# Performance work log

Measured on AMD Instinct MI355X. Metric: run time of the kernel, lower is better.

Reference implementation:

```python
import jax, jax.numpy as jnp
import numpy as np
from jax import lax

D = 30   # embedding_dim (hardcoded in repo)
Q = 30   # question length
N = 4000 # number of sentences in doc
S = 100  # tokens per sentence
K = 5    # k_for_maxpool
SLOPE = 0.1  # LeakyReLU negative slope


def setup_inputs() -> dict:
    key = jax.random.key(0)
    ks = jax.random.split(key, 20)
    rn = lambda k, sh: jax.random.normal(k, sh, dtype=jnp.float32)
    ru = lambda k, sh: jax.random.uniform(k, sh, dtype=jnp.float32)
    return {
        "doc_sents_embeds": rn(ks[0], (N, S, D)),
        "sents_gaf": ru(ks[1], (N, 3)),
        "question_embeds": rn(ks[2], (Q, D)),
        "q_idfs": ru(ks[3], (Q, 1)),
        "doc_gaf": ru(ks[4], (4,)),
        "conv1_w": rn(ks[5], (D, D, 3)) * 0.1,
        "conv1_b": rn(ks[6], (D,)) * 0.1,
        "conv2_w": rn(ks[7], (D, D, 3)) * 0.1,
        "conv2_b": rn(ks[8], (D,)) * 0.1,
        "qw_W": rn(ks[9], (1, D + 1)) * 0.1,
        "qw_b": rn(ks[10], (1,)) * 0.1,
        "lq1_W": rn(ks[11], (8, 6)) * 0.1,
        "lq1_b": rn(ks[12], (8,)) * 0.1,
        "lq2_W": rn(ks[13], (1, 8)) * 0.1,
        "lq2_b": rn(ks[14], (1,)) * 0.1,
        "so_W": rn(ks[15], (1, 4)) * 0.1,
        "so_b": rn(ks[16], (1,)) * 0.1,
        "fl_W": rn(ks[17], (1, 5)) * 0.1,
        "fl_b": rn(ks[18], (1,)) * 0.1,
    }


def _leaky(x):
    return jnp.where(x >= 0, x, SLOPE * x)


def _conv_block(x, w, b):
    # x: [B, L, D]. torch Conv1d(D, D, 3, padding=2) then slice [1:L+1]
    # is exactly a 'same' conv with padding 1 on each side; then residual add.
    y = lax.conv_general_dilated(x.transpose(0, 2, 1), w, (1,), [(1, 1)],
                                 dimension_numbers=("NCH", "OIH", "NCH"))
    y = _leaky(y + b[None, :, None])
    return y.transpose(0, 2, 1) + x


def _cos_sim(A, B):
    # A: [Q, D], B: [N, S, D] -> [N, Q, S] (num/den as in torch my_cosine_sim)
    num = jnp.einsum("qd,nsd->nqs", A, B)
    den = jnp.linalg.norm(A, axis=-1)[None, :, None] * jnp.linalg.norm(B, axis=-1)[:, None, :]
    return num / den


def _pool(sim):
    # sort-based k-max pooling -> [max, avg_of_top_k]; sim: [N, Q, S] -> [N, Q, 2]
    vals = lax.top_k(sim, K)[0]  # descending
    return jnp.stack([vals[..., 0], vals.mean(-1)], axis=-1)


def reference(doc_sents_embeds, sents_gaf, question_embeds, q_idfs, doc_gaf,
              conv1_w, conv1_b, conv2_w, conv2_b, qw_W, qw_b,
              lq1_W, lq1_b, lq2_W, lq2_b, so_W, so_b, fl_W, fl_b):
    # question context (two residual trigram convs)
    q_conv = _conv_block(question_embeds[None], conv1_w, conv1_b)
    q_conv = _conv_block(q_conv, conv2_w, conv2_b)[0]          # [Q, D]
    # question term weights
    qw_in = jnp.concatenate([q_conv, q_idfs], axis=-1)          # [Q, D+1]
    q_weights = jax.nn.softmax((qw_in @ qw_W.T + qw_b)[:, 0])   # [Q]
    # sentence context convs (batched over all sentences)
    conv_res = _conv_block(doc_sents_embeds, conv1_w, conv1_b)
    conv_res = _conv_block(conv_res, conv2_w, conv2_b)          # [N, S, D]
    # similarity matrices
    sim_insens = _cos_sim(question_embeds, doc_sents_embeds)    # [N, Q, S]
    sim_oh = (sim_insens > 1.0 - 1e-3).astype(sim_insens.dtype)
    sim_sens = _cos_sim(q_conv, conv_res)
    # k-max pooling and per-q tiny MLP attention
    feats = jnp.concatenate([_pool(sim_oh), _pool(sim_insens), _pool(sim_sens)], axis=-1)  # [N, Q, 6]
    lo = _leaky(feats @ lq1_W.T + lq1_b) @ lq2_W.T + lq2_b      # [N, Q, 1]
    lo = lo[..., 0] * q_weights[None, :]
    sent_emit = lo.sum(-1) / Q                                  # [N]
    # per-sentence output layer
    sent_feats = jnp.concatenate([sents_gaf, sent_emit[:, None]], axis=-1)  # [N, 4]
    sent_scores = jax.nn.sigmoid((sent_feats @ so_W.T + so_b)[:, 0])        # [N]
    # doc-level score
    doc_rep = jnp.concatenate([jnp.max(sent_scores)[None], doc_gaf])        # [5]
    final = doc_rep @ fl_W.T + fl_b                                          # [1]
    return final, sent_scores
```

## Files before the change

kernel.cpp:

```cpp
#include <hip/hip_runtime.h>
#include <hip/hip_bf16.h>

#define SLOPE 0.1f

#define OFF_QW    1816
#define OFF_QNI   1846
#define OFF_QNS   1876
#define OFF_QNN   1906
#define OFF_B1    4606
#define OFF_B2    7336
#define OFF_LQ1W  7366
#define OFF_LQ1B  7414
#define OFF_LQ2W  7422
#define OFF_LQ2B  7430
#define OFF_SOW   7431
#define OFF_SOB   7435
#define OFF_FLW   7436
#define OFF_FLB   7441
#define U16_QEA   16384
#define U16_QCA   17408
#define U16_WB1   18432
#define U16_WB2   21504

#define XDW 1548

typedef __attribute__((ext_vector_type(8))) __bf16 bf16x8;
typedef __attribute__((ext_vector_type(4))) float f32x4;

union Frag { uint4 u4; uint u[4]; bf16x8 v; };

__device__ __forceinline__ float bf2f(ushort h) {
    union { uint u; float f; } c; c.u = ((uint)h) << 16; return c.f;
}
__device__ __forceinline__ ushort f2bf(float f) {
    union { float f; uint u; } c; c.f = f;
    uint u = c.u;
    return (ushort)((u + 0x7FFFu + ((u >> 16) & 1u)) >> 16);
}
__device__ __forceinline__ float ldx(const void* p, long i, int bf) {
    if (bf) return bf2f(((const ushort*)p)[i]);
    return ((const float*)p)[i];
}
__device__ __forceinline__ uint pk2(float lo, float hi) {
    uint r;
    asm("v_cvt_pk_bf16_f32 %0, %1, %2" : "=v"(r) : "v"(lo), "v"(hi));
    return r;
}
__device__ __forceinline__ float blo(uint u) { return __uint_as_float(u << 16); }
__device__ __forceinline__ float bhi(uint u) { return __uint_as_float(u & 0xFFFF0000u); }
__device__ __forceinline__ float lk(float x) { return fmaxf(x, SLOPE * x); }

#define CE(x, y) { float _hi = fmaxf(x, y), _lo = fminf(x, y); x = _hi; y = _lo; }

__device__ __forceinline__ void sort4d(float& a, float& b, float& c, float& d) {
    CE(a, b); CE(c, d); CE(a, c); CE(b, d); CE(b, c);
}
__device__ __forceinline__ void merge44_5(const float* a, const float* b, float* t) {
    t[0] = fmaxf(a[0], b[0]);
    t[1] = fmaxf(fminf(a[0], b[0]), fmaxf(a[1], b[1]));
    t[2] = fmaxf(fmaxf(fminf(a[0], b[1]), fminf(a[1], b[0])), fmaxf(a[2], b[2]));
    t[3] = fmaxf(fmaxf(fminf(a[0], b[2]), fminf(a[1], b[1])),
                 fmaxf(fminf(a[2], b[0]), fmaxf(a[3], b[3])));
    t[4] = fmaxf(fmaxf(fminf(a[0], b[3]), fminf(a[1], b[2])),
                 fmaxf(fminf(a[2], b[1]), fminf(a[3], b[0])));
}
__device__ __forceinline__ void merge54_5(const float* a, const float* b, float* t) {
    t[0] = fmaxf(a[0], b[0]);
    t[1] = fmaxf(fminf(a[0], b[0]), fmaxf(a[1], b[1]));
    t[2] = fmaxf(fmaxf(fminf(a[0], b[1]), fminf(a[1], b[0])), fmaxf(a[2], b[2]));
    t[3] = fmaxf(fmaxf(fminf(a[0], b[2]), fminf(a[1], b[1])),
                 fmaxf(fminf(a[2], b[0]), fmaxf(a[3], b[3])));
    t[4] = fmaxf(fmaxf(fmaxf(fminf(a[0], b[3]), fminf(a[1], b[2])),
                       fmaxf(fminf(a[2], b[1]), fminf(a[3], b[0]))), a[4]);
}
__device__ __forceinline__ void merge55_5(const float* a, const float* b, float* t) {
    t[0] = fmaxf(a[0], b[0]);
    t[1] = fmaxf(fminf(a[0], b[0]), fmaxf(a[1], b[1]));
    t[2] = fmaxf(fmaxf(fminf(a[0], b[1]), fminf(a[1], b[0])), fmaxf(a[2], b[2]));
    t[3] = fmaxf(fmaxf(fminf(a[0], b[2]), fminf(a[1], b[1])),
                 fmaxf(fminf(a[2], b[0]), fmaxf(a[3], b[3])));
    t[4] = fmaxf(fmaxf(fmaxf(fminf(a[0], b[3]), fminf(a[1], b[2])),
                       fmaxf(fminf(a[2], b[1]), fminf(a[3], b[0]))),
                 fmaxf(a[4], b[4]));
}

__device__ __forceinline__ int detect_bf(const void* doc_in, int tid, int* scnt) {
    if (tid == 0) *scnt = 0;
    __syncthreads();
    const ushort* p = (const ushort*)doc_in;
    int local = 0;
    for (int i = tid; i < 4096; i += 256) {
        unsigned e = (p[i] >> 7) & 0xFFu;
        if (e != 0u && (e < 100u || e > 134u)) local++;
    }
    atomicAdd(scnt, local);
    __syncthreads();
    return (*scnt > 200) ? 0 : 1;
}

__global__ __launch_bounds__(256) void k_prep(
        const void* doc_in,
        const void* qe_in, const void* qidf_in,
        const void* w1_in, const void* b1_in,
        const void* w2_in, const void* b2_in,
        const void* qwW_in, const void* qwb_in,
        const void* lq1W_in, const void* lq1b_in,
        const void* lq2W_in, const void* lq2b_in,
        const void* soW_in, const void* sob_in,
        const void* flW_in, const void* flb_in,
        float* ws) {
    const int tid = threadIdx.x;
    const int blk = blockIdx.x;
    __shared__ float QE[900], T1[900], QC[900], W[2700], IDF[32], LG[32];
    __shared__ int scnt;

    const int bf = detect_bf(doc_in, tid, &scnt);
    ushort* wsu = (ushort*)ws;

    if (blk == 1) {
        if (tid == 0) { ((int*)ws)[0] = bf; }
        if (tid < 30) ws[OFF_B1 + tid] = ldx(b1_in, tid, bf);
        if (tid < 48) ws[OFF_LQ1W + tid] = ldx(lq1W_in, tid, bf);
        if (tid < 8)  { ws[OFF_LQ1B + tid] = ldx(lq1b_in, tid, bf);
                        ws[OFF_LQ2W + tid] = ldx(lq2W_in, tid, bf); }
        if (tid < 4)  ws[OFF_SOW + tid] = ldx(soW_in, tid, bf);
        if (tid < 5)  ws[OFF_FLW + tid] = ldx(flW_in, tid, bf);
        if (tid == 1) { ws[OFF_LQ2B] = ldx(lq2b_in, 0, bf);
                        ws[OFF_SOB]  = ldx(sob_in, 0, bf);
                        ws[OFF_FLB]  = ldx(flb_in, 0, bf); }
        for (int i = tid; i < 3072; i += 256) {
            int o = i / 96, kk = i % 96;
            int k = kk >> 5, ii = kk & 31;
            float v1 = 0.f;
            if (o < 30 && ii < 30) v1 = ldx(w1_in, (long)o*90 + ii*3 + k, bf);
            wsu[U16_WB1 + i] = f2bf(v1);
        }
        return;
    }
    if (blk == 2) {
        if (tid < 30) ws[OFF_B2 + tid] = ldx(b2_in, tid, bf);
        for (int i = tid; i < 3072; i += 256) {
            int o = i / 96, kk = i % 96;
            int k = kk >> 5, ii = kk & 31;
            float v2 = 0.f;
            if (o < 30 && ii < 30) v2 = ldx(w2_in, (long)o*90 + ii*3 + k, bf);
            wsu[U16_WB2 + i] = f2bf(v2);
        }
        return;
    }

    if (tid == 0) { ((int*)ws)[0] = bf; }

    for (int i = tid; i < 900; i += 256) QE[i] = ldx(qe_in, i, bf);
    if (tid < 30) IDF[tid] = ldx(qidf_in, tid, bf);
    for (int i = tid; i < 2700; i += 256) W[i] = ldx(w1_in, i, bf);
    __syncthreads();

    for (int idx = tid; idx < 900; idx += 256) {
        int s = idx / 30, o = idx % 30;
        float acc = ldx(b1_in, o, bf);
        for (int k = 0; k < 3; ++k) {
            int t = s + k - 1;
            if (t < 0 || t >= 30) continue;
            for (int i = 0; i < 30; ++i) acc += QE[t*30 + i] * W[o*90 + i*3 + k];
        }
        acc = acc >= 0.f ? acc : SLOPE * acc;
        T1[idx] = acc + QE[idx];
    }
    __syncthreads();
    for (int i = tid; i < 2700; i += 256) W[i] = ldx(w2_in, i, bf);
    __syncthreads();
    for (int idx = tid; idx < 900; idx += 256) {
        int s = idx / 30, o = idx % 30;
        float acc = ldx(b2_in, o, bf);
        for (int k = 0; k < 3; ++k) {
            int t = s + k - 1;
            if (t < 0 || t >= 30) continue;
            for (int i = 0; i < 30; ++i) acc += T1[t*30 + i] * W[o*90 + i*3 + k];
        }
        acc = acc >= 0.f ? acc : SLOPE * acc;
        QC[idx] = acc + T1[idx];
    }
    __syncthreads();

    if (tid < 30) {
        float s1 = 0.f, s2 = 0.f;
        for (int d = 0; d < 30; ++d) {
            float a = QE[tid*30 + d]; s1 += a*a;
            float b = QC[tid*30 + d]; s2 += b*b;
        }
        float n1 = sqrtf(s1);
        ws[OFF_QNN + tid] = n1;
        ws[OFF_QNI + tid] = 1.0f / n1;
        ws[OFF_QNS + tid] = 1.0f / sqrtf(s2);
        float z = ldx(qwb_in, 0, bf);
        for (int d = 0; d < 30; ++d) z += QC[tid*30 + d] * ldx(qwW_in, d, bf);
        z += IDF[tid] * ldx(qwW_in, 30, bf);
        LG[tid] = z;
    }
    __syncthreads();
    if (tid == 0) {
        float m = -1e30f;
        for (int q = 0; q < 30; ++q) m = fmaxf(m, LG[q]);
        float sum = 0.f, e[30];
        for (int q = 0; q < 30; ++q) { e[q] = expf(LG[q] - m); sum += e[q]; }
        for (int q = 0; q < 30; ++q) ws[OFF_QW + q] = e[q] / sum;
    }
    for (int i = tid; i < 1024; i += 256) {
        int q = i >> 5, d = i & 31;
        float ve = (q < 30 && d < 30) ? QE[q*30 + d] : 0.f;
        float vc = (q < 30 && d < 30) ? QC[q*30 + d] : 0.f;
        wsu[U16_QEA + i] = f2bf(ve);
        wsu[U16_QCA + i] = f2bf(vc);
    }
}

__global__ __launch_bounds__(128, 4) void k_main(const void* doc_in, const void* gaf_in,
                                                 void* out, float* ws) {
    const int n = blockIdx.x;
    const int tid = threadIdx.x;
    const int bf = ((const int*)ws)[0];
    const int lane = tid & 63;
    const int wid = tid >> 6;
    const int l15 = lane & 15;
    const int quad = lane >> 4;
    const int q = wid * 16 + l15;

    __shared__ __align__(16) uint XA[XDW];
    __shared__ __align__(16) uint XB[XDW];
    __shared__ __align__(16) float INVX[112];
    __shared__ float PART[2];

    const ushort* wsu = (const ushort*)ws;
    const uint4* qeA = (const uint4*)(wsu + U16_QEA);
    const uint4* qcA = (const uint4*)(wsu + U16_QCA);
    const uint4* wb1 = (const uint4*)(wsu + U16_WB1);
    const uint4* wb2 = (const uint4*)(wsu + U16_WB2);

    float ga0 = ldx(gaf_in, (long)n*3 + 0, bf);
    float ga1 = ldx(gaf_in, (long)n*3 + 1, bf);
    float ga2 = ldx(gaf_in, (long)n*3 + 2, bf);

    if (tid < 48) {
        int j = (tid < 15) ? tid : (1500 + tid);
        XA[j] = 0u; XB[j] = 0u;
    } else if (tid < 60) {
        INVX[100 + (tid - 48)] = 0.f;
    }
    for (int g = tid; g < 400; g += 128) {
        int r = g >> 2, t = g & 3;
        int base = (r + 1) * 15 + t * 4;
        float s2;
        if (bf) {
            const uint* gp = (const uint*)doc_in + (size_t)n * 1500 + r * 15 + t * 4;
            uint a = gp[0], b = gp[1], c = gp[2];
            uint d = (t < 3) ? gp[3] : 0u;
            XA[base] = a; XA[base + 1] = b; XA[base + 2] = c;
            if (t < 3) XA[base + 3] = d;
            float x0 = blo(a), x1 = bhi(a), x2 = blo(b), x3 = bhi(b);
            float x4 = blo(c), x5 = bhi(c), x6 = blo(d), x7 = bhi(d);
            s2 = x0*x0 + x1*x1 + x2*x2 + x3*x3 + x4*x4 + x5*x5 + x6*x6 + x7*x7;
        } else {
            const float* p = (const float*)doc_in + (size_t)n * 3000 + r * 30 + t * 8;
            float2 f0 = ((const float2*)p)[0];
            float2 f1 = ((const float2*)p)[1];
            float2 f2 = ((const float2*)p)[2];
            float2 f3 = (t < 3) ? ((const float2*)p)[3] : make_float2(0.f, 0.f);
            XA[base]     = pk2(f0.x, f0.y);
            XA[base + 1] = pk2(f1.x, f1.y);
            XA[base + 2] = pk2(f2.x, f2.y);
            if (t < 3) XA[base + 3] = pk2(f3.x, f3.y);
            s2 = f0.x*f0.x + f0.y*f0.y + f1.x*f1.x + f1.y*f1.y
               + f2.x*f2.x + f2.y*f2.y + f3.x*f3.x + f3.y*f3.y;
        }
        s2 += __shfl_xor(s2, 1);
        s2 += __shfl_xor(s2, 2);
        if (t == 0) INVX[r] = 1.f / sqrtf(s2);
    }
    __syncthreads();

    auto sim_pool = [&](const uint4* qa, int iqOff, bool do_oh,
                        float& o0, float& o1, float& m0, float& m1) {
        Frag b;
        b.u4 = qa[q * 4 + quad];
        f32x4 acc[7];
        #pragma unroll
        for (int mt = 0; mt < 7; ++mt) {
            int m = mt * 16 + l15;
            Frag a;
            if (m < 100) {
                int base = (m + 1) * 15 + quad * 4;
                a.u[0] = XA[base];     a.u[1] = XA[base + 1];
                a.u[2] = XA[base + 2]; a.u[3] = XA[base + 3];
            } else { a.u[0] = a.u[1] = a.u[2] = a.u[3] = 0u; }
            f32x4 z = {0.f, 0.f, 0.f, 0.f};
            acc[mt] = __builtin_amdgcn_mfma_f32_16x16x32_bf16(a.v, b.v, z, 0, 0, 0);
        }
        const float4* INVX4 = (const float4*)INVX;
        float thr = (do_oh && q < 30) ? 0.999f * ws[OFF_QNN + q] : 1e30f;
        float iq  = (q < 30) ? ws[iqOff + q] : 0.f;
        float g[7][4];
        int cnt = 0;
        #pragma unroll
        for (int mt = 0; mt < 7; ++mt) {
            float4 ix = INVX4[mt * 4 + quad];
            float ixa[4] = {ix.x, ix.y, ix.z, ix.w};
            #pragma unroll
            for (int r = 0; r < 4; ++r) {
                float u = acc[mt][r] * ixa[r];
                if (mt == 6 && (quad * 4 + r) >= 4) u = -1e30f;
                g[mt][r] = u;
                if (do_oh) cnt += (u > thr) ? 1 : 0;
            }
        }
        #pragma unroll
        for (int mt = 0; mt < 7; ++mt) sort4d(g[mt][0], g[mt][1], g[mt][2], g[mt][3]);
        float p0[5], p1[5], p2[5], q0[5], q1[5], t[5];
        merge44_5(g[0], g[1], p0);
        merge44_5(g[2], g[3], p1);
        merge44_5(g[4], g[5], p2);
        merge55_5(p0, p1, q0);
        merge54_5(p2, g[6], q1);
        merge55_5(q0, q1, t);
        #pragma unroll
        for (int d = 16; d < 64; d <<= 1) {
            float pp[5];
            pp[0] = __shfl_xor(t[0], d); pp[1] = __shfl_xor(t[1], d);
            pp[2] = __shfl_xor(t[2], d); pp[3] = __shfl_xor(t[3], d);
            pp[4] = __shfl_xor(t[4], d);
            if (do_oh) cnt += __shfl_xor(cnt, d);
            float tn[5];
            merge55_5(t, pp, tn);
            t[0] = tn[0]; t[1] = tn[1]; t[2] = tn[2]; t[3] = tn[3]; t[4] = tn[4];
        }
        if (do_oh) {
            o0 = cnt > 0 ? 1.f : 0.f;
            o1 = (float)(cnt > 5 ? 5 : cnt) * 0.2f;
        }
        m0 = t[0] * iq;
        m1 = (t[0] + t[1] + t[2] + t[3] + t[4]) * 0.2f * iq;
    };

    auto conv_dual = [&](const uint* src, uint* dst, const uint4* wb, int bOff,
                         bool donorm) {
        const int mtb = wid ? 3 : 0;
        const int mte = wid ? 6 : 2;
        Frag wf0[3], wf1[3];
        #pragma unroll
        for (int k = 0; k < 3; ++k) {
            wf0[k].u4 = wb[l15 * 12 + k * 4 + quad];
            wf1[k].u4 = wb[(16 + l15) * 12 + k * 4 + quad];
        }
        float b40[4], b41[4];
        #pragma unroll
        for (int r = 0; r < 4; ++r) {
            int o0 = quad * 4 + r, o1 = 16 + o0;
            b40[r] = ws[bOff + o0];
            b41[r] = (o1 < 30) ? ws[bOff + o1] : 0.f;
        }
        for (int mt = mtb; mt <= mte; ++mt) {
            const int s = mt * 16 + l15;
            const bool sv = (s < 100);
            Frag f0, f1, f2;
            if (sv) {
                int base = s * 15 + quad * 4;
                f0.u[0] = src[base];      f0.u[1] = src[base + 1];
                f0.u[2] = src[base + 2];  f0.u[3] = src[base + 3];
                base += 15;
                f1.u[0] = src[base];      f1.u[1] = src[base + 1];
                f1.u[2] = src[base + 2];  f1.u[3] = src[base + 3];
                base += 15;
                f2.u[0] = src[base];      f2.u[1] = src[base + 1];
                f2.u[2] = src[base + 2];  f2.u[3] = src[base + 3];
            } else {
                f0.u[0]=f0.u[1]=f0.u[2]=f0.u[3]=0u;
                f1 = f0; f2 = f0;
            }
            const int db = (s + 1) * 15 + quad * 2;
            uint u0 = 0u, u1 = 0u, u2 = 0u, u3 = 0u;
            if (sv) {
                uint2 ua = *(const uint2*)(src + db);
                uint2 ub = *(const uint2*)(src + db + 8);
                u0 = ua.x; u1 = ua.y; u2 = ub.x; u3 = ub.y;
            }
            f32x4 a0 = {0.f, 0.f, 0.f, 0.f}, a1 = {0.f, 0.f, 0.f, 0.f};
            a0 = __builtin_amdgcn_mfma_f32_16x16x32_bf16(wf0[0].v, f0.v, a0, 0, 0, 0);
            a1 = __builtin_amdgcn_mfma_f32_16x16x32_bf16(wf1[0].v, f0.v, a1, 0, 0, 0);
            a0 = __builtin_amdgcn_mfma_f32_16x16x32_bf16(wf0[1].v, f1.v, a0, 0, 0, 0);
            a1 = __builtin_amdgcn_mfma_f32_16x16x32_bf16(wf1[1].v, f1.v, a1, 0, 0, 0);
            a0 = __builtin_amdgcn_mfma_f32_16x16x32_bf16(wf0[2].v, f2.v, a0, 0, 0, 0);
            a1 = __builtin_amdgcn_mfma_f32_16x16x32_bf16(wf1[2].v, f2.v, a1, 0, 0, 0);
            float ss = 0.f;
            if (sv) {
                float v0 = lk(a0[0] + b40[0]) + blo(u0);
                float v1 = lk(a0[1] + b40[1]) + bhi(u0);
                float v2 = lk(a0[2] + b40[2]) + blo(u1);
                float v3 = lk(a0[3] + b40[3]) + bhi(u1);
                *(uint2*)(dst + db) = make_uint2(pk2(v0, v1), pk2(v2, v3));
                float w0 = lk(a1[0] + b41[0]) + blo(u2);
                float w1 = lk(a1[1] + b41[1]) + bhi(u2);
                uint s45 = pk2(w0, w1);
                ss = v0*v0 + v1*v1 + v2*v2 + v3*v3 + w0*w0 + w1*w1;
                if (quad < 3) {
                    float w2 = lk(a1[2] + b41[2]) + blo(u3);
                    float w3 = lk(a1[3] + b41[3]) + bhi(u3);
                    *(uint2*)(dst + db + 8) = make_uint2(s45, pk2(w2, w3));
                    ss += w2*w2 + w3*w3;
                } else {
                    dst[db + 8] = s45;
                }
            }
            if (donorm) {
                ss += __shfl_xor(ss, 16);
                ss += __shfl_xor(ss, 32);
                if (quad == 0 && sv) INVX[s] = 1.f / sqrtf(ss);
            }
        }
    };

    float fe0, fe1, fe2, fe3, fe4, fe5;
    sim_pool(qeA, OFF_QNI, true, fe0, fe1, fe2, fe3);
    conv_dual(XA, XB, wb1, OFF_B1, false);
    __syncthreads();

    conv_dual(XB, XA, wb2, OFF_B2, true);
    __syncthreads();

    sim_pool(qcA, OFF_QNS, false, fe0, fe1, fe4, fe5);
    float val = 0.f;
    if (quad == 0 && q < 30) {
        float f[6] = {fe0, fe1, fe2, fe3, fe4, fe5};
        float lo = ws[OFF_LQ2B];
        #pragma unroll
        for (int j = 0; j < 8; ++j) {
            float h = ws[OFF_LQ1B + j];
            #pragma unroll
            for (int i = 0; i < 6; ++i) h += f[i] * ws[OFF_LQ1W + j*6 + i];
            h = lk(h);
            lo += h * ws[OFF_LQ2W + j];
        }
        val = lo * ws[OFF_QW + q];
    }
    #pragma unroll
    for (int d = 32; d >= 1; d >>= 1) val += __shfl_xor(val, d);
    if (lane == 0) PART[wid] = val;
    __syncthreads();

    if (tid == 0) {
        float emit = (PART[0] + PART[1]) * (1.f / 30.f);
        float z = ws[OFF_SOB];
        z += ga0 * ws[OFF_SOW + 0];
        z += ga1 * ws[OFF_SOW + 1];
        z += ga2 * ws[OFF_SOW + 2];
        z += emit * ws[OFF_SOW + 3];
        float sc = 1.f / (1.f + expf(-z));
        if (bf) ((__hip_bfloat16*)out)[1 + n] = __float2bfloat16(sc);
        else    ((float*)out)[1 + n] = sc;
    }
}

__global__ __launch_bounds__(256) void k_final(const void* docgaf_in, void* out, const float* ws) {
    const int tid = threadIdx.x;
    const int bf = ((const int*)ws)[0];
    __shared__ float red[256];
    float m = -1e30f;
    for (int i = tid; i < 4000; i += 256) {
        float v = bf ? __bfloat162float(((const __hip_bfloat16*)out)[1 + i])
                     : ((const float*)out)[1 + i];
        m = fmaxf(m, v);
    }
    red[tid] = m;
    __syncthreads();
    for (int off = 128; off > 0; off >>= 1) {
        if (tid < off) red[tid] = fmaxf(red[tid], red[tid + off]);
        __syncthreads();
    }
    if (tid == 0) {
        float f = ws[OFF_FLB] + red[0] * ws[OFF_FLW + 0];
        for (int i = 0; i < 4; ++i) f += ldx(docgaf_in, i, bf) * ws[OFF_FLW + 1 + i];
        if (bf) ((__hip_bfloat16*)out)[0] = __float2bfloat16(f);
        else    ((float*)out)[0] = f;
    }
}

extern "C" void kernel_launch(void* const* d_in, const int* in_sizes, int n_in,
                              void* d_out, int out_size, void* d_ws, size_t ws_size,
                              hipStream_t stream) {
    float* ws = (float*)d_ws;
    k_prep<<<3, 256, 0, stream>>>(d_in[0], d_in[2], d_in[3], d_in[5], d_in[6], d_in[7], d_in[8],
                                  d_in[9], d_in[10], d_in[11], d_in[12], d_in[13], d_in[14],
                                  d_in[15], d_in[16], d_in[17], d_in[18], ws);
    k_main<<<4000, 128, 0, stream>>>(d_in[0], d_in[1], d_out, ws);
    k_final<<<1, 256, 0, stream>>>(d_in[4], d_out, ws);
}
```

Before: 184.1 us.

## Cut register pressure in main kernel and coalesce document load

Raises the k_main occupancy target from 4 to 6 blocks per SM. To fit that budget, the k-max pooling becomes a streaming merge per MFMA tile, so the seven accumulator tiles no longer stay live. Conv weight fragments are reloaded per output tile instead of held in registers, conv tiles are interleaved across the two waves, and the doc load uses contiguous 16-byte vector loads with a separate pass for row norms. Pooled features now go through shared memory and one wave finishes the MLP, which adds an extra barrier plus repeated weight loads from global or cache.

```diff
diff --git a/kernel.cpp b/kernel.cpp
--- a/kernel.cpp
+++ b/kernel.cpp
@@ -55,15 +55,6 @@
 __device__ __forceinline__ void sort4d(float& a, float& b, float& c, float& d) {
     CE(a, b); CE(c, d); CE(a, c); CE(b, d); CE(b, c);
 }
-__device__ __forceinline__ void merge44_5(const float* a, const float* b, float* t) {
-    t[0] = fmaxf(a[0], b[0]);
-    t[1] = fmaxf(fminf(a[0], b[0]), fmaxf(a[1], b[1]));
-    t[2] = fmaxf(fmaxf(fminf(a[0], b[1]), fminf(a[1], b[0])), fmaxf(a[2], b[2]));
-    t[3] = fmaxf(fmaxf(fminf(a[0], b[2]), fminf(a[1], b[1])),
-                 fmaxf(fminf(a[2], b[0]), fmaxf(a[3], b[3])));
-    t[4] = fmaxf(fmaxf(fminf(a[0], b[3]), fminf(a[1], b[2])),
-                 fmaxf(fminf(a[2], b[1]), fminf(a[3], b[0])));
-}
 __device__ __forceinline__ void merge54_5(const float* a, const float* b, float* t) {
     t[0] = fmaxf(a[0], b[0]);
     t[1] = fmaxf(fminf(a[0], b[0]), fmaxf(a[1], b[1]));
@@ -215,7 +206,7 @@
     }
 }
 
-__global__ __launch_bounds__(128, 4) void k_main(const void* doc_in, const void* gaf_in,
+__global__ __launch_bounds__(128, 6) void k_main(const void* doc_in, const void* gaf_in,
                                                  void* out, float* ws) {
     const int n = blockIdx.x;
     const int tid = threadIdx.x;
@@ -224,12 +215,11 @@
     const int wid = tid >> 6;
     const int l15 = lane & 15;
     const int quad = lane >> 4;
-    const int q = wid * 16 + l15;
 
     __shared__ __align__(16) uint XA[XDW];
     __shared__ __align__(16) uint XB[XDW];
     __shared__ __align__(16) float INVX[112];
-    __shared__ float PART[2];
+    __shared__ float FE[30][6];
 
     const ushort* wsu = (const ushort*)ws;
     const uint4* qeA = (const uint4*)(wsu + U16_QEA);
@@ -247,43 +237,47 @@
     } else if (tid < 60) {
         INVX[100 + (tid - 48)] = 0.f;
     }
-    for (int g = tid; g < 400; g += 128) {
-        int r = g >> 2, t = g & 3;
-        int base = (r + 1) * 15 + t * 4;
-        float s2;
-        if (bf) {
-            const uint* gp = (const uint*)doc_in + (size_t)n * 1500 + r * 15 + t * 4;
-            uint a = gp[0], b = gp[1], c = gp[2];
-            uint d = (t < 3) ? gp[3] : 0u;
-            XA[base] = a; XA[base + 1] = b; XA[base + 2] = c;
-            if (t < 3) XA[base + 3] = d;
-            float x0 = blo(a), x1 = bhi(a), x2 = blo(b), x3 = bhi(b);
-            float x4 = blo(c), x5 = bhi(c), x6 = blo(d), x7 = bhi(d);
-            s2 = x0*x0 + x1*x1 + x2*x2 + x3*x3 + x4*x4 + x5*x5 + x6*x6 + x7*x7;
-        } else {
-            const float* p = (const float*)doc_in + (size_t)n * 3000 + r * 30 + t * 8;
-            float2 f0 = ((const float2*)p)[0];
-            float2 f1 = ((const float2*)p)[1];
-            float2 f2 = ((const float2*)p)[2];
-            float2 f3 = (t < 3) ? ((const float2*)p)[3] : make_float2(0.f, 0.f);
-            XA[base]     = pk2(f0.x, f0.y);
-            XA[base + 1] = pk2(f1.x, f1.y);
-            XA[base + 2] = pk2(f2.x, f2.y);
-            if (t < 3) XA[base + 3] = pk2(f3.x, f3.y);
-            s2 = f0.x*f0.x + f0.y*f0.y + f1.x*f1.x + f1.y*f1.y
-               + f2.x*f2.x + f2.y*f2.y + f3.x*f3.x + f3.y*f3.y;
-        }
-        s2 += __shfl_xor(s2, 1);
-        s2 += __shfl_xor(s2, 2);
-        if (t == 0) INVX[r] = 1.f / sqrtf(s2);
-    }
-    __syncthreads();
-
-    auto sim_pool = [&](const uint4* qa, int iqOff, bool do_oh,
-                        float& o0, float& o1, float& m0, float& m1) {
+    if (bf) {
+        const uint4* g = (const uint4*)((const ushort*)doc_in + (size_t)n * 3000);
+        for (int j = tid; j < 375; j += 128) {
+            uint4 v = g[j];
+            int d = 15 + 4 * j;
+            XA[d] = v.x; XA[d + 1] = v.y; XA[d + 2] = v.z; XA[d + 3] = v.w;
+        }
+    } else {
+        const float4* p4 = (const float4*)((const float*)doc_in + (size_t)n * 3000);
+        for (int j = tid; j < 750; j += 128) {
+            float4 f = p4[j];
+            int d = 15 + 2 * j;
+            XA[d]     = pk2(f.x, f.y);
+            XA[d + 1] = pk2(f.z, f.w);
+        }
+    }
+    __syncthreads();
+
+    if (tid < 100) {
+        const uint* r = XA + (tid + 1) * 15;
+        float s = 0.f;
+        #pragma unroll
+        for (int i = 0; i < 15; ++i) {
+            uint u = r[i];
+            float lo = __uint_as_float(u << 16);
+            float hi = __uint_as_float(u & 0xFFFF0000u);
+            s += lo * lo + hi * hi;
+        }
+        INVX[tid] = 1.f / sqrtf(s);
+    }
+    __syncthreads();
+
+    auto sim_pool = [&](const uint4* qa, int iqOff, int fbase, bool do_oh) {
+        const int q = wid * 16 + l15;
         Frag b;
         b.u4 = qa[q * 4 + quad];
-        f32x4 acc[7];
+        const float4* INVX4 = (const float4*)INVX;
+        float thr = (do_oh && q < 30) ? 0.999f * ws[OFF_QNN + q] : 1e30f;
+        float iq  = (q < 30) ? ws[iqOff + q] : 0.f;
+        float t[5] = {-1e30f, -1e30f, -1e30f, -1e30f, -1e30f};
+        int cnt = 0;
         #pragma unroll
         for (int mt = 0; mt < 7; ++mt) {
             int m = mt * 16 + l15;
@@ -294,34 +288,26 @@
                 a.u[2] = XA[base + 2]; a.u[3] = XA[base + 3];
             } else { a.u[0] = a.u[1] = a.u[2] = a.u[3] = 0u; }
             f32x4 z = {0.f, 0.f, 0.f, 0.f};
-            acc[mt] = __builtin_amdgcn_mfma_f32_16x16x32_bf16(a.v, b.v, z, 0, 0, 0);
-        }
-        const float4* INVX4 = (const float4*)INVX;
-        float thr = (do_oh && q < 30) ? 0.999f * ws[OFF_QNN + q] : 1e30f;
-        float iq  = (q < 30) ? ws[iqOff + q] : 0.f;
-        float g[7][4];
-        int cnt = 0;
-        #pragma unroll
-        for (int mt = 0; mt < 7; ++mt) {
+            f32x4 acc = __builtin_amdgcn_mfma_f32_16x16x32_bf16(a.v, b.v, z, 0, 0, 0);
             float4 ix = INVX4[mt * 4 + quad];
-            float ixa[4] = {ix.x, ix.y, ix.z, ix.w};
-            #pragma unroll
-            for (int r = 0; r < 4; ++r) {
-                float u = acc[mt][r] * ixa[r];
-                if (mt == 6 && (quad * 4 + r) >= 4) u = -1e30f;
-                g[mt][r] = u;
-                if (do_oh) cnt += (u > thr) ? 1 : 0;
-            }
-        }
-        #pragma unroll
-        for (int mt = 0; mt < 7; ++mt) sort4d(g[mt][0], g[mt][1], g[mt][2], g[mt][3]);
-        float p0[5], p1[5], p2[5], q0[5], q1[5], t[5];
-        merge44_5(g[0], g[1], p0);
-        merge44_5(g[2], g[3], p1);
-        merge44_5(g[4], g[5], p2);
-        merge55_5(p0, p1, q0);
-        merge54_5(p2, g[6], q1);
-        merge55_5(q0, q1, t);
+            float g0 = acc[0] * ix.x, g1 = acc[1] * ix.y;
+            float g2 = acc[2] * ix.z, g3 = acc[3] * ix.w;
+            if (mt == 6) {
+                if (quad * 4 + 0 >= 4) g0 = -1e30f;
+                if (quad * 4 + 1 >= 4) g1 = -1e30f;
+                if (quad * 4 + 2 >= 4) g2 = -1e30f;
+                if (quad * 4 + 3 >= 4) g3 = -1e30f;
+            }
+            if (do_oh) {
+                cnt += (g0 > thr) ? 1 : 0; cnt += (g1 > thr) ? 1 : 0;
+                cnt += (g2 > thr) ? 1 : 0; cnt += (g3 > thr) ? 1 : 0;
+            }
+            sort4d(g0, g1, g2, g3);
+            float ga[4] = {g0, g1, g2, g3};
+            float tn[5];
+            merge54_5(t, ga, tn);
+            t[0] = tn[0]; t[1] = tn[1]; t[2] = tn[2]; t[3] = tn[3]; t[4] = tn[4];
+        }
         #pragma unroll
         for (int d = 16; d < 64; d <<= 1) {
             float pp[5];
@@ -333,24 +319,18 @@
             merge55_5(t, pp, tn);
             t[0] = tn[0]; t[1] = tn[1]; t[2] = tn[2]; t[3] = tn[3]; t[4] = tn[4];
         }
-        if (do_oh) {
-            o0 = cnt > 0 ? 1.f : 0.f;
-            o1 = (float)(cnt > 5 ? 5 : cnt) * 0.2f;
-        }
-        m0 = t[0] * iq;
-        m1 = (t[0] + t[1] + t[2] + t[3] + t[4]) * 0.2f * iq;
+        if (quad == 0 && q < 30) {
+            if (do_oh) {
+                FE[q][0] = cnt > 0 ? 1.f : 0.f;
+                FE[q][1] = (float)(cnt > 5 ? 5 : cnt) * 0.2f;
+            }
+            FE[q][fbase]     = t[0] * iq;
+            FE[q][fbase + 1] = (t[0] + t[1] + t[2] + t[3] + t[4]) * 0.2f * iq;
+        }
     };
 
     auto conv_dual = [&](const uint* src, uint* dst, const uint4* wb, int bOff,
                          bool donorm) {
-        const int mtb = wid ? 3 : 0;
-        const int mte = wid ? 6 : 2;
-        Frag wf0[3], wf1[3];
-        #pragma unroll
-        for (int k = 0; k < 3; ++k) {
-            wf0[k].u4 = wb[l15 * 12 + k * 4 + quad];
-            wf1[k].u4 = wb[(16 + l15) * 12 + k * 4 + quad];
-        }
         float b40[4], b41[4];
         #pragma unroll
         for (int r = 0; r < 4; ++r) {
@@ -358,7 +338,9 @@
             b40[r] = ws[bOff + o0];
             b41[r] = (o1 < 30) ? ws[bOff + o1] : 0.f;
         }
-        for (int mt = mtb; mt <= mte; ++mt) {
+        const int nmt = wid ? 3 : 4;
+        for (int i = 0; i < nmt; ++i) {
+            const int mt = wid + 2 * i;
             const int s = mt * 16 + l15;
             const bool sv = (s < 100);
             Frag f0, f1, f2;
@@ -376,38 +358,37 @@
                 f0.u[0]=f0.u[1]=f0.u[2]=f0.u[3]=0u;
                 f1 = f0; f2 = f0;
             }
-            const int db = (s + 1) * 15 + quad * 2;
-            uint u0 = 0u, u1 = 0u, u2 = 0u, u3 = 0u;
-            if (sv) {
-                uint2 ua = *(const uint2*)(src + db);
-                uint2 ub = *(const uint2*)(src + db + 8);
-                u0 = ua.x; u1 = ua.y; u2 = ub.x; u3 = ub.y;
-            }
-            f32x4 a0 = {0.f, 0.f, 0.f, 0.f}, a1 = {0.f, 0.f, 0.f, 0.f};
-            a0 = __builtin_amdgcn_mfma_f32_16x16x32_bf16(wf0[0].v, f0.v, a0, 0, 0, 0);
-            a1 = __builtin_amdgcn_mfma_f32_16x16x32_bf16(wf1[0].v, f0.v, a1, 0, 0, 0);
-            a0 = __builtin_amdgcn_mfma_f32_16x16x32_bf16(wf0[1].v, f1.v, a0, 0, 0, 0);
-            a1 = __builtin_amdgcn_mfma_f32_16x16x32_bf16(wf1[1].v, f1.v, a1, 0, 0, 0);
-            a0 = __builtin_amdgcn_mfma_f32_16x16x32_bf16(wf0[2].v, f2.v, a0, 0, 0, 0);
-            a1 = __builtin_amdgcn_mfma_f32_16x16x32_bf16(wf1[2].v, f2.v, a1, 0, 0, 0);
             float ss = 0.f;
-            if (sv) {
-                float v0 = lk(a0[0] + b40[0]) + blo(u0);
-                float v1 = lk(a0[1] + b40[1]) + bhi(u0);
-                float v2 = lk(a0[2] + b40[2]) + blo(u1);
-                float v3 = lk(a0[3] + b40[3]) + bhi(u1);
-                *(uint2*)(dst + db) = make_uint2(pk2(v0, v1), pk2(v2, v3));
-                float w0 = lk(a1[0] + b41[0]) + blo(u2);
-                float w1 = lk(a1[1] + b41[1]) + bhi(u2);
-                uint s45 = pk2(w0, w1);
-                ss = v0*v0 + v1*v1 + v2*v2 + v3*v3 + w0*w0 + w1*w1;
-                if (quad < 3) {
-                    float w2 = lk(a1[2] + b41[2]) + blo(u3);
-                    float w3 = lk(a1[3] + b41[3]) + bhi(u3);
-                    *(uint2*)(dst + db + 8) = make_uint2(s45, pk2(w2, w3));
-                    ss += w2*w2 + w3*w3;
-                } else {
-                    dst[db + 8] = s45;
+            #pragma unroll
+            for (int nt = 0; nt < 2; ++nt) {
+                f32x4 acc = {0.f, 0.f, 0.f, 0.f};
+                {
+                    Frag wf;
+                    wf.u4 = wb[(nt * 16 + l15) * 12 + 0 * 4 + quad];
+                    acc = __builtin_amdgcn_mfma_f32_16x16x32_bf16(wf.v, f0.v, acc, 0, 0, 0);
+                    wf.u4 = wb[(nt * 16 + l15) * 12 + 1 * 4 + quad];
+                    acc = __builtin_amdgcn_mfma_f32_16x16x32_bf16(wf.v, f1.v, acc, 0, 0, 0);
+                    wf.u4 = wb[(nt * 16 + l15) * 12 + 2 * 4 + quad];
+                    acc = __builtin_amdgcn_mfma_f32_16x16x32_bf16(wf.v, f2.v, acc, 0, 0, 0);
+                }
+                if (sv) {
+                    const float* b4 = nt ? b41 : b40;
+                    const int db = (s + 1) * 15 + nt * 8 + quad * 2;
+                    if (nt == 0 || quad < 3) {
+                        uint2 ua = *(const uint2*)(src + db);
+                        float v0 = lk(acc[0] + b4[0]) + blo(ua.x);
+                        float v1 = lk(acc[1] + b4[1]) + bhi(ua.x);
+                        float v2 = lk(acc[2] + b4[2]) + blo(ua.y);
+                        float v3 = lk(acc[3] + b4[3]) + bhi(ua.y);
+                        *(uint2*)(dst + db) = make_uint2(pk2(v0, v1), pk2(v2, v3));
+                        ss += v0*v0 + v1*v1 + v2*v2 + v3*v3;
+                    } else {
+                        uint u = src[db];
+                        float v0 = lk(acc[0] + b4[0]) + blo(u);
+                        float v1 = lk(acc[1] + b4[1]) + bhi(u);
+                        dst[db] = pk2(v0, v1);
+                        ss += v0*v0 + v1*v1;
+                    }
                 }
             }
             if (donorm) {
@@ -418,44 +399,43 @@
         }
     };
 
-    float fe0, fe1, fe2, fe3, fe4, fe5;
-    sim_pool(qeA, OFF_QNI, true, fe0, fe1, fe2, fe3);
+    sim_pool(qeA, OFF_QNI, 2, true);
     conv_dual(XA, XB, wb1, OFF_B1, false);
     __syncthreads();
 
     conv_dual(XB, XA, wb2, OFF_B2, true);
     __syncthreads();
 
-    sim_pool(qcA, OFF_QNS, false, fe0, fe1, fe4, fe5);
-    float val = 0.f;
-    if (quad == 0 && q < 30) {
-        float f[6] = {fe0, fe1, fe2, fe3, fe4, fe5};
-        float lo = ws[OFF_LQ2B];
+    sim_pool(qcA, OFF_QNS, 4, false);
+    __syncthreads();
+
+    if (wid == 0) {
+        float val = 0.f;
+        if (lane < 30) {
+            float lo = ws[OFF_LQ2B];
+            #pragma unroll
+            for (int j = 0; j < 8; ++j) {
+                float h = ws[OFF_LQ1B + j];
+                #pragma unroll
+                for (int f = 0; f < 6; ++f) h += FE[lane][f] * ws[OFF_LQ1W + j*6 + f];
+                h = lk(h);
+                lo += h * ws[OFF_LQ2W + j];
+            }
+            val = lo * ws[OFF_QW + lane];
+        }
         #pragma unroll
-        for (int j = 0; j < 8; ++j) {
-            float h = ws[OFF_LQ1B + j];
-            #pragma unroll
-            for (int i = 0; i < 6; ++i) h += f[i] * ws[OFF_LQ1W + j*6 + i];
-            h = lk(h);
-            lo += h * ws[OFF_LQ2W + j];
-        }
-        val = lo * ws[OFF_QW + q];
-    }
-    #pragma unroll
-    for (int d = 32; d >= 1; d >>= 1) val += __shfl_xor(val, d);
-    if (lane == 0) PART[wid] = val;
-    __syncthreads();
-
-    if (tid == 0) {
-        float emit = (PART[0] + PART[1]) * (1.f / 30.f);
-        float z = ws[OFF_SOB];
-        z += ga0 * ws[OFF_SOW + 0];
-        z += ga1 * ws[OFF_SOW + 1];
-        z += ga2 * ws[OFF_SOW + 2];
-        z += emit * ws[OFF_SOW + 3];
-        float sc = 1.f / (1.f + expf(-z));
-        if (bf) ((__hip_bfloat16*)out)[1 + n] = __float2bfloat16(sc);
-        else    ((float*)out)[1 + n] = sc;
+        for (int d = 32; d >= 1; d >>= 1) val += __shfl_xor(val, d);
+        if (lane == 0) {
+            float emit = val * (1.f / 30.f);
+            float z = ws[OFF_SOB];
+            z += ga0 * ws[OFF_SOW + 0];
+            z += ga1 * ws[OFF_SOW + 1];
+            z += ga2 * ws[OFF_SOW + 2];
+            z += emit * ws[OFF_SOW + 3];
+            float sc = 1.f / (1.f + expf(-z));
+            if (bf) ((__hip_bfloat16*)out)[1 + n] = __float2bfloat16(sc);
+            else    ((float*)out)[1 + n] = sc;
+        }
     }
 }
 
```

New measurement: 181.2 us. No clear change (-1.6%).
